# Optimization experiments

Hardware: AMD Instinct MI355X
Metric: run time of the kernel (lower is better)

The kernel has to match this reference:

```python
import jax, jax.numpy as jnp
import numpy as np

D_MODEL = 1024
NUM_HEADS = 16
D_FF = 2688
BATCH = 2
SEQ = 2048
EPS = 1e-5


def _trunc_normal(key, shape, std):
    # truncated normal on [-3, 3] then scaled by std (matches trunc_normal_(mean=0,std,a=-3,b=3) approximately)
    return std * jax.random.truncated_normal(key, -3.0 / std if std > 0 else -3.0, 3.0 / std if std > 0 else 3.0, shape, jnp.float32) * std / std if False else jax.random.truncated_normal(key, -3.0, 3.0, shape, jnp.float32) * std


def setup_inputs() -> dict:
    key = jax.random.key(0)
    ks = jax.random.split(key, 8)
    def lin(k, d_out, d_in):
        std = (2.0 / (d_in + d_out)) ** 0.5
        return _trunc_normal(k, (d_out, d_in), std)
    return {
        "x": jax.random.normal(ks[0], (BATCH, SEQ, D_MODEL), jnp.float32),
        "wqkv": lin(ks[1], 3 * D_MODEL, D_MODEL),
        "wo": lin(ks[2], D_MODEL, D_MODEL),
        "g1": jnp.ones((D_MODEL,), jnp.float32),
        "g2": jnp.ones((D_MODEL,), jnp.float32),
        "w1": lin(ks[3], D_FF, D_MODEL),
        "w2": lin(ks[4], D_MODEL, D_FF),
        "w3": lin(ks[5], D_FF, D_MODEL),
    }


def _rmsnorm(x, g):
    rms = jnp.sqrt(jnp.mean(x * x, axis=-1, keepdims=True) + EPS)
    return x * (g / rms)


def _mhsa(x, wqkv, wo):
    B, S, D = x.shape
    H, Dk = NUM_HEADS, D // NUM_HEADS
    qkv = jnp.einsum('bsd,ed->bse', x, wqkv)  # [B,S,3D]
    q, k, v = jnp.split(qkv, 3, axis=-1)
    def heads(t):
        return t.reshape(B, S, H, Dk).transpose(0, 2, 1, 3)  # [B,H,S,Dk]
    q, k, v = heads(q), heads(k), heads(v)
    scores = jnp.einsum('bhqd,bhkd->bhqk', q, k) / jnp.sqrt(jnp.asarray(Dk, x.dtype))
    causal = jnp.tril(jnp.ones((S, S), bool))
    scores = jnp.where(causal, scores, -jnp.inf)
    attn = jax.nn.softmax(scores, axis=-1)
    out = jnp.einsum('bhqk,bhkd->bhqd', attn, v)
    out = out.transpose(0, 2, 1, 3).reshape(B, S, D)
    return jnp.einsum('bsd,ed->bse', out, wo)


def _swiglu(x, w1, w2, w3):
    a = jnp.einsum('bsd,fd->bsf', x, w1)
    b = jnp.einsum('bsd,fd->bsf', x, w3)
    h = (a * jax.nn.sigmoid(a)) * b
    return jnp.einsum('bsf,df->bsd', h, w2)


def reference(x, wqkv, wo, g1, g2, w1, w2, w3):
    x = x + _mhsa(_rmsnorm(x, g1), wqkv, wo)
    x = x + _swiglu(_rmsnorm(x, g2), w1, w2, w3)
    return x
```

## Files before the change

### kernel.cpp

```cpp
#include <hip/hip_runtime.h>
#include <cstdint>
#include <cstddef>

typedef unsigned short u16;
typedef __attribute__((ext_vector_type(8))) short short8;
typedef __attribute__((ext_vector_type(4))) float float4v;

struct alignas(8) u16x4 { u16 x, y, z, w; };

__device__ __forceinline__ float bf2f(u16 u) {
  union { uint32_t i; float f; } x;
  x.i = ((uint32_t)u) << 16;
  return x.f;
}
__device__ __forceinline__ u16 f2bf(float f) {
  union { float f; uint32_t i; } x;
  x.f = f;
  uint32_t r = x.i + 0x7fffu + ((x.i >> 16) & 1u);
  return (u16)(r >> 16);
}
__device__ __forceinline__ int4 pack8(const float4& a, const float4& b) {
  int4 r;
  r.x = (uint32_t)f2bf(a.x) | ((uint32_t)f2bf(a.y) << 16);
  r.y = (uint32_t)f2bf(a.z) | ((uint32_t)f2bf(a.w) << 16);
  r.z = (uint32_t)f2bf(b.x) | ((uint32_t)f2bf(b.y) << 16);
  r.w = (uint32_t)f2bf(b.z) | ((uint32_t)f2bf(b.w) << 16);
  return r;
}

__device__ __forceinline__ void gload_lds16(const void* g, void* l) {
  __builtin_amdgcn_global_load_lds(
      (const __attribute__((address_space(1))) void*)g,
      (__attribute__((address_space(3))) void*)l, 16, 0, 0);
}

__device__ __forceinline__ int2 xcd_swizzle_xmajor() {
  const int gx = gridDim.x, gy = gridDim.y;
  const int nwg = gx * gy;
  const int lin = blockIdx.x + blockIdx.y * gx;
  const int nl = (lin & 7) * (nwg >> 3) + (lin >> 3);
  const int bx = nl / gy;
  const int by = nl - bx * gy;
  return make_int2(bx, by);
}

struct PrepArgs {
  const float* src[5];
  u16* dst[5];
  int pre[6];
};

__global__ __launch_bounds__(256) void prep_kernel(PrepArgs a)
{
  const int g = blockIdx.x * 256 + threadIdx.x;
  if (g >= a.pre[5]) return;
  int t = 0;
#pragma unroll
  for (int i = 0; i < 5; i++) if (g >= a.pre[i + 1]) t = i + 1;
  const int idx = (g - a.pre[t]) * 8;
  const float* s = a.src[t] + idx;
  float4 v0 = *(const float4*)(s);
  float4 v1 = *(const float4*)(s + 4);
  *(int4*)(a.dst[t] + idx) = pack8(v0, v1);
}

template <int RMODE, bool OUTF32, int TN>
__global__ __launch_bounds__(256) void gemm_bt_kernel(
    const u16* __restrict__ A, const u16* __restrict__ B,
    void* __restrict__ Cv, const void* __restrict__ Rv,
    int M, int N, int K)
{
  constexpr int JN = TN / 32;
  __shared__ u16 As[2][128 * 32];
  __shared__ u16 Bs[2][TN * 32];
  const int t = threadIdx.x;
  const int lane = t & 63;
  const int wave = t >> 6;
  const int l15 = lane & 15;
  const int quad = lane >> 4;
  const int wm = (wave >> 1) * 64;
  const int wn = (wave & 1) * (TN / 2);
  const int2 bb = xcd_swizzle_xmajor();
  const int m0 = bb.y * 128;
  const int n0 = bb.x * TN;
  const int sw = quad ^ ((l15 >> 1) & 3);

  float4v acc[4][JN] = {};

  const int r0 = t >> 2, q0s = (t & 3) ^ ((t >> 3) & 3);
  const int s1 = 256 + t;
  const int r1 = s1 >> 2, q1s = (s1 & 3) ^ ((s1 >> 3) & 3);

  auto stage = [&](int bi, int kk) {
    gload_lds16(A + (size_t)(m0 + r0) * K + kk + q0s * 8, &As[bi][(wave * 64) * 8]);
    gload_lds16(A + (size_t)(m0 + r1) * K + kk + q1s * 8, &As[bi][(256 + wave * 64) * 8]);
    gload_lds16(B + (size_t)(n0 + r0) * K + kk + q0s * 8, &Bs[bi][(wave * 64) * 8]);
    if (TN == 128)
      gload_lds16(B + (size_t)(n0 + r1) * K + kk + q1s * 8, &Bs[bi][(256 + wave * 64) * 8]);
  };
  auto compute = [&](int bi) {
    short8 af[4], bfr[JN];
#pragma unroll
    for (int i = 0; i < 4; i++)
      af[i] = *(const short8*)(&As[bi][((wm + i * 16 + l15) * 4 + sw) * 8]);
#pragma unroll
    for (int j = 0; j < JN; j++)
      bfr[j] = *(const short8*)(&Bs[bi][((wn + j * 16 + l15) * 4 + sw) * 8]);
#pragma unroll
    for (int i = 0; i < 4; i++)
#pragma unroll
      for (int j = 0; j < JN; j++)
        acc[i][j] = __builtin_amdgcn_mfma_f32_16x16x32_bf16(af[i], bfr[j], acc[i][j], 0, 0, 0);
  };

  stage(0, 0);
  __syncthreads();
  for (int kk = 0; kk < K; kk += 64) {
    stage(1, kk + 32);
    compute(0);
    __syncthreads();
    if (kk + 64 < K) stage(0, kk + 64);
    compute(1);
    __syncthreads();
  }

#pragma unroll
  for (int i = 0; i < 4; i++) {
#pragma unroll
    for (int r = 0; r < 4; r++) {
      const int row = m0 + wm + i * 16 + quad * 4 + r;
      const size_t base = (size_t)row * N;
#pragma unroll
      for (int j = 0; j < JN; j++) {
        const int col = n0 + wn + j * 16 + l15;
        float v = acc[i][j][r];
        if (RMODE == 1) v += ((const float*)Rv)[base + col];
        if (RMODE == 2) v += bf2f(((const u16*)Rv)[base + col]);
        if (OUTF32) ((float*)Cv)[base + col] = v;
        else        ((u16*)Cv)[base + col] = f2bf(v);
      }
    }
  }
}

__global__ __launch_bounds__(256) void gemm_w13_kernel(
    const u16* __restrict__ A, const u16* __restrict__ B1,
    const u16* __restrict__ B2, u16* __restrict__ C,
    int M, int N, int K)
{
  __shared__ u16 As[2][128 * 32];
  __shared__ u16 B1s[2][64 * 32];
  __shared__ u16 B2s[2][64 * 32];
  const int t = threadIdx.x;
  const int lane = t & 63;
  const int wave = t >> 6;
  const int l15 = lane & 15;
  const int quad = lane >> 4;
  const int wm = (wave >> 1) * 64;
  const int wn = (wave & 1) * 32;
  const int2 bb = xcd_swizzle_xmajor();
  const int m0 = bb.y * 128;
  const int n0 = bb.x * 64;
  const int sw = quad ^ ((l15 >> 1) & 3);

  float4v accA[4][2] = {};
  float4v accB[4][2] = {};

  const int r0 = t >> 2, q0s = (t & 3) ^ ((t >> 3) & 3);
  const int s1 = 256 + t;
  const int r1 = s1 >> 2, q1s = (s1 & 3) ^ ((s1 >> 3) & 3);

  auto stage = [&](int bi, int kk) {
    gload_lds16(A + (size_t)(m0 + r0) * K + kk + q0s * 8, &As[bi][(wave * 64) * 8]);
    gload_lds16(A + (size_t)(m0 + r1) * K + kk + q1s * 8, &As[bi][(256 + wave * 64) * 8]);
    gload_lds16(B1 + (size_t)(n0 + r0) * K + kk + q0s * 8, &B1s[bi][(wave * 64) * 8]);
    gload_lds16(B2 + (size_t)(n0 + r0) * K + kk + q0s * 8, &B2s[bi][(wave * 64) * 8]);
  };
  auto compute = [&](int bi) {
    short8 af[4], b1f[2], b2f[2];
#pragma unroll
    for (int i = 0; i < 4; i++)
      af[i] = *(const short8*)(&As[bi][((wm + i * 16 + l15) * 4 + sw) * 8]);
#pragma unroll
    for (int j = 0; j < 2; j++) {
      b1f[j] = *(const short8*)(&B1s[bi][((wn + j * 16 + l15) * 4 + sw) * 8]);
      b2f[j] = *(const short8*)(&B2s[bi][((wn + j * 16 + l15) * 4 + sw) * 8]);
    }
#pragma unroll
    for (int i = 0; i < 4; i++)
#pragma unroll
      for (int j = 0; j < 2; j++) {
        accA[i][j] = __builtin_amdgcn_mfma_f32_16x16x32_bf16(af[i], b1f[j], accA[i][j], 0, 0, 0);
        accB[i][j] = __builtin_amdgcn_mfma_f32_16x16x32_bf16(af[i], b2f[j], accB[i][j], 0, 0, 0);
      }
  };

  stage(0, 0);
  __syncthreads();
  for (int kk = 0; kk < K; kk += 64) {
    stage(1, kk + 32);
    compute(0);
    __syncthreads();
    if (kk + 64 < K) stage(0, kk + 64);
    compute(1);
    __syncthreads();
  }

#pragma unroll
  for (int i = 0; i < 4; i++) {
#pragma unroll
    for (int r = 0; r < 4; r++) {
      const int row = m0 + wm + i * 16 + quad * 4 + r;
      const size_t base = (size_t)row * N;
#pragma unroll
      for (int j = 0; j < 2; j++) {
        const int col = n0 + wn + j * 16 + l15;
        float a = accA[i][j][r];
        float b = accB[i][j][r];
        float h = a / (1.f + __expf(-a)) * b;
        C[base + col] = f2bf(h);
      }
    }
  }
}

__global__ __launch_bounds__(256) void vtrans_kernel(
    const u16* __restrict__ qkv, u16* __restrict__ VtG)
{
  __shared__ u16 T[64 * 72];
  const int t = threadIdx.x;
  const int s0 = blockIdx.x * 64;
  const int bh = blockIdx.y, b = bh >> 4, h = bh & 15;
  {
    const int sl = t >> 2, dseg = (t & 3) * 16;
    const size_t src = ((size_t)b * 2048 + s0 + sl) * 3072 + 2048 + h * 64 + dseg;
    int4 v0 = *(const int4*)(qkv + src);
    int4 v1 = *(const int4*)(qkv + src + 8);
    *(int4*)(&T[sl * 72 + dseg]) = v0;
    *(int4*)(&T[sl * 72 + dseg + 8]) = v1;
  }
  __syncthreads();
  {
    const int d = t >> 2, sseg = (t & 3) * 16;
    alignas(16) u16 buf[16];
#pragma unroll
    for (int i = 0; i < 16; i++) buf[i] = T[(sseg + i) * 72 + d];
    u16* dst = VtG + ((size_t)bh * 64 + d) * 2048 + s0 + sseg;
    *(int4*)(dst) = *(const int4*)(&buf[0]);
    *(int4*)(dst + 8) = *(const int4*)(&buf[8]);
  }
}

__global__ __launch_bounds__(256) void attn_kernel(
    const u16* __restrict__ qkv, const u16* __restrict__ VtG,
    u16* __restrict__ outp)
{
  __shared__ u16 Ks[2][128 * 32];
  __shared__ u16 Vt[4][64 * 32];
  __shared__ u16 Pl[4][2048];
  const int t = threadIdx.x;
  const int lane = t & 63;
  const int wave = t >> 6;
  const int l15 = lane & 15;
  const int quad = lane >> 4;
  const int sw = quad ^ ((l15 >> 1) & 3);
  const int gx = gridDim.x;
  const int nwg = gx * gridDim.y;
  const int lin = blockIdx.x + blockIdx.y * gx;
  const int nl = (lin & 7) * (nwg >> 3) + (lin >> 3);
  const int bh = nl / gx;
  const int pair = nl - bh * gx;
  const int b = bh >> 4, h = bh & 15;
  const size_t srow = (size_t)b * 2048;
  const int rr = lane >> 2, qs = (lane & 3) ^ ((lane >> 3) & 3);
  u16* plw = Pl[wave];

  for (int tsel = 0; tsel < 2; tsel++) {
    const int qt = tsel ? 31 - pair : pair;
    const int tq0 = qt * 64;
    const int q = tq0 + wave * 16 + l15;

    short8 qf[2];
    {
      const size_t qbase = (srow + q) * 3072 + h * 64;
#pragma unroll
      for (int dh = 0; dh < 2; dh++) {
        int4 raw = *(const int4*)(qkv + qbase + dh * 32 + quad * 8);
        const u16* rp = (const u16*)&raw;
        short8 f;
#pragma unroll
        for (int j = 0; j < 8; j++)
          ((u16*)&f)[j] = f2bf(bf2f(rp[j]) * 0.125f);
        qf[dh] = f;
      }
    }

    float m_i = -INFINITY, l_i = 0.f;
    float4v accO[4] = {};
    const int nc = (qt + 2) >> 1;

    for (int ic = 0; ic < nc; ic++) {
      const int c0 = ic * 128;
#pragma unroll
      for (int k = 0; k < 8; k++) {
        const int I = wave * 8 + k;
        if (I < 16) {
          const int half = I >> 3, rb = (I & 7) * 16, row = rb + rr;
          gload_lds16(qkv + (srow + c0 + row) * 3072 + 1024 + h * 64 + half * 32 + qs * 8,
                      &Ks[half][rb * 32]);
        } else {
          const int g = (I - 16) >> 2, rb = ((I - 16) & 3) * 16, row = rb + rr;
          gload_lds16(VtG + ((size_t)bh * 64 + row) * 2048 + c0 + g * 32 + qs * 8,
                      &Vt[g][rb * 32]);
        }
      }
      __syncthreads();

      float4v accS[8];
#pragma unroll
      for (int ks = 0; ks < 8; ks++) {
        short8 kf0 = *(const short8*)(&Ks[0][((ks * 16 + l15) * 4 + sw) * 8]);
        short8 kf1 = *(const short8*)(&Ks[1][((ks * 16 + l15) * 4 + sw) * 8]);
        float4v z = {};
        z = __builtin_amdgcn_mfma_f32_16x16x32_bf16(kf0, qf[0], z, 0, 0, 0);
        accS[ks] = __builtin_amdgcn_mfma_f32_16x16x32_bf16(kf1, qf[1], z, 0, 0, 0);
      }

      if (ic == nc - 1) {
#pragma unroll
        for (int ks = 0; ks < 8; ks++)
#pragma unroll
          for (int r = 0; r < 4; r++)
            if (c0 + ks * 16 + quad * 4 + r > q) accS[ks][r] = -INFINITY;
      }

      float cmax = -INFINITY;
#pragma unroll
      for (int ks = 0; ks < 8; ks++)
#pragma unroll
        for (int r = 0; r < 4; r++) cmax = fmaxf(cmax, accS[ks][r]);
      cmax = fmaxf(cmax, __shfl_xor(cmax, 16));
      cmax = fmaxf(cmax, __shfl_xor(cmax, 32));
      const float mn = fmaxf(m_i, cmax);
      const float alpha = __expf(m_i - mn);

      float psum = 0.f;
#pragma unroll
      for (int ks = 0; ks < 8; ks++) {
        float p0 = __expf(accS[ks][0] - mn);
        float p1 = __expf(accS[ks][1] - mn);
        float p2 = __expf(accS[ks][2] - mn);
        float p3 = __expf(accS[ks][3] - mn);
        psum += (p0 + p1) + (p2 + p3);
        u16x4 pk;
        pk.x = f2bf(p0); pk.y = f2bf(p1); pk.z = f2bf(p2); pk.w = f2bf(p3);
        const int seg = ((ks & 1) * 2 + (quad >> 1)) ^ ((l15 >> 1) & 3);
        *(u16x4*)(&plw[(ks >> 1) * 512 + (l15 * 4 + seg) * 8 + (quad & 1) * 4]) = pk;
      }
      psum += __shfl_xor(psum, 16);
      psum += __shfl_xor(psum, 32);
      l_i = l_i * alpha + psum;
      m_i = mn;
#pragma unroll
      for (int ds = 0; ds < 4; ds++)
#pragma unroll
        for (int r = 0; r < 4; r++) accO[ds][r] *= alpha;

      __threadfence_block();

#pragma unroll
      for (int kh = 0; kh < 4; kh++) {
        short8 pf = *(const short8*)(&plw[kh * 512 + (l15 * 4 + sw) * 8]);
#pragma unroll
        for (int ds = 0; ds < 4; ds++) {
          short8 vf = *(const short8*)(&Vt[kh][((ds * 16 + l15) * 4 + sw) * 8]);
          accO[ds] = __builtin_amdgcn_mfma_f32_16x16x32_bf16(vf, pf, accO[ds], 0, 0, 0);
        }
      }
      __syncthreads();
    }

    const float invl = 1.f / l_i;
    const size_t obase = (srow + q) * 1024 + h * 64;
#pragma unroll
    for (int ds = 0; ds < 4; ds++) {
      u16x4 pk;
      pk.x = f2bf(accO[ds][0] * invl);
      pk.y = f2bf(accO[ds][1] * invl);
      pk.z = f2bf(accO[ds][2] * invl);
      pk.w = f2bf(accO[ds][3] * invl);
      *(u16x4*)(outp + obase + ds * 16 + quad * 4) = pk;
    }
  }
}

template <bool XF32>
__global__ __launch_bounds__(256) void rmsnorm_kernel(
    const void* __restrict__ xv, const float* __restrict__ g, u16* __restrict__ o)
{
  const int row = blockIdx.x;
  const int t = threadIdx.x;
  float f0, f1, f2, f3;
  if (XF32) {
    float4 v = *(const float4*)((const float*)xv + (size_t)row * 1024 + t * 4);
    f0 = v.x; f1 = v.y; f2 = v.z; f3 = v.w;
  } else {
    int2 v = *(const int2*)((const u16*)xv + (size_t)row * 1024 + t * 4);
    const u16* p = (const u16*)&v;
    f0 = bf2f(p[0]); f1 = bf2f(p[1]); f2 = bf2f(p[2]); f3 = bf2f(p[3]);
  }
  float ss = f0 * f0 + f1 * f1 + f2 * f2 + f3 * f3;
#pragma unroll
  for (int off = 32; off > 0; off >>= 1) ss += __shfl_down(ss, off);
  __shared__ float red[4];
  if ((t & 63) == 0) red[t >> 6] = ss;
  __syncthreads();
  const float tot = red[0] + red[1] + red[2] + red[3];
  const float inv = rsqrtf(tot * (1.0f / 1024.0f) + 1e-5f);
  float4 gv = *(const float4*)(g + t * 4);
  u16x4 ov;
  ov.x = f2bf(f0 * gv.x * inv);
  ov.y = f2bf(f1 * gv.y * inv);
  ov.z = f2bf(f2 * gv.z * inv);
  ov.w = f2bf(f3 * gv.w * inv);
  *(u16x4*)(o + (size_t)row * 1024 + t * 4) = ov;
}

extern "C" void kernel_launch(void* const* d_in, const int* in_sizes, int n_in,
                              void* d_out, int out_size, void* d_ws, size_t ws_size,
                              hipStream_t stream)
{
  const float* x    = (const float*)d_in[0];
  const float* wqkv = (const float*)d_in[1];
  const float* wo   = (const float*)d_in[2];
  const float* g1   = (const float*)d_in[3];
  const float* g2   = (const float*)d_in[4];
  const float* w1   = (const float*)d_in[5];
  const float* w2   = (const float*)d_in[6];
  const float* w3   = (const float*)d_in[7];
  float* out = (float*)d_out;
  char* ws = (char*)d_ws;
  (void)in_sizes; (void)n_in; (void)out_size; (void)ws_size;

  size_t off = 0;
  auto alloc = [&](size_t bytes) { void* p = ws + off; off += (bytes + 255) & ~(size_t)255; return p; };
  u16* wqkvb = (u16*)alloc((size_t)3072 * 1024 * 2);
  u16* wob   = (u16*)alloc((size_t)1024 * 1024 * 2);
  u16* w1b   = (u16*)alloc((size_t)2688 * 1024 * 2);
  u16* w2b   = (u16*)alloc((size_t)2688 * 1024 * 2);
  u16* w3b   = (u16*)alloc((size_t)2688 * 1024 * 2);
  u16* S1    = (u16*)alloc((size_t)4096 * 1024 * 2);
  u16* S2    = (u16*)alloc((size_t)4096 * 3072 * 2);
  u16* S3    = (u16*)alloc((size_t)4096 * 1024 * 2);
  u16* VtG   = (u16*)alloc((size_t)32 * 64 * 2048 * 2);

  PrepArgs pa;
  const float* srcs[5] = {wqkv, wo, w1, w2, w3};
  u16* dsts[5] = {wqkvb, wob, w1b, w2b, w3b};
  const int nelem[5] = {3072 * 1024, 1024 * 1024, 2688 * 1024, 2688 * 1024, 2688 * 1024};
  int pre = 0;
  for (int i = 0; i < 5; i++) {
    pa.src[i] = srcs[i];
    pa.dst[i] = dsts[i];
    pa.pre[i] = pre;
    pre += nelem[i] / 8;
  }
  pa.pre[5] = pre;
  prep_kernel<<<(pre + 255) / 256, 256, 0, stream>>>(pa);

  rmsnorm_kernel<true><<<4096, 256, 0, stream>>>(x, g1, S1);
  gemm_bt_kernel<0, false, 128><<<dim3(24, 32), 256, 0, stream>>>(S1, wqkvb, S2,
                                                  nullptr, 4096, 3072, 1024);
  vtrans_kernel<<<dim3(32, 32), 256, 0, stream>>>(S2, VtG);
  attn_kernel<<<dim3(16, 32), 256, 0, stream>>>(S2, VtG, S1);
  gemm_bt_kernel<1, false, 64><<<dim3(16, 32), 256, 0, stream>>>(S1, wob, S3, x,
                                                  4096, 1024, 1024);
  rmsnorm_kernel<false><<<4096, 256, 0, stream>>>(S3, g2, S1);
  gemm_w13_kernel<<<dim3(42, 32), 256, 0, stream>>>(S1, w1b, w3b, S2,
                                                  4096, 2688, 1024);
  gemm_bt_kernel<2, true, 64><<<dim3(16, 32), 256, 0, stream>>>(S2, w2b, out, S3,
                                                  4096, 1024, 2688);
}
```

Before: 339.6 us.

## Triple-buffer GEMM K-loop and double-buffer attention KV with partial vmcnt waits

The GEMM and fused W1/W3 kernels move from a two-stage LDS pipeline to three stages. Each iteration issues the load two steps ahead and waits with an explicit s_waitcnt vmcnt count, so only the oldest tile must arrive before the barrier. The attention kernel double-buffers its K and V tiles, prefetching the next chunk while computing the current one. This should hide global-to-LDS latency in exchange for more LDS per block, which may lower occupancy, and it relies on hand-counted vmcnt values being correct.

```diff
diff --git a/kernel.cpp b/kernel.cpp
--- a/kernel.cpp
+++ b/kernel.cpp
@@ -33,6 +33,20 @@
       (const __attribute__((address_space(1))) void*)g,
       (__attribute__((address_space(3))) void*)l, 16, 0, 0);
 }
+
+#define WAITV_BAR(N)                                              \
+  do {                                                            \
+    asm volatile("s_waitcnt vmcnt(%0)" ::"n"(N) : "memory");      \
+    __builtin_amdgcn_s_barrier();                                 \
+    __builtin_amdgcn_sched_barrier(0);                            \
+  } while (0)
+
+#define BAR_ONLY()                                                \
+  do {                                                            \
+    __builtin_amdgcn_sched_barrier(0);                            \
+    __builtin_amdgcn_s_barrier();                                 \
+    __builtin_amdgcn_sched_barrier(0);                            \
+  } while (0)
 
 __device__ __forceinline__ int2 xcd_swizzle_xmajor() {
   const int gx = gridDim.x, gy = gridDim.y;
@@ -71,8 +85,9 @@
     int M, int N, int K)
 {
   constexpr int JN = TN / 32;
-  __shared__ u16 As[2][128 * 32];
-  __shared__ u16 Bs[2][TN * 32];
+  constexpr int NLD = (TN == 128) ? 4 : 3;
+  __shared__ u16 As[3][128 * 32];
+  __shared__ u16 Bs[3][TN * 32];
   const int t = threadIdx.x;
   const int lane = t & 63;
   const int wave = t >> 6;
@@ -113,16 +128,23 @@
         acc[i][j] = __builtin_amdgcn_mfma_f32_16x16x32_bf16(af[i], bfr[j], acc[i][j], 0, 0, 0);
   };
 
+  const int nk = K >> 5;
   stage(0, 0);
-  __syncthreads();
-  for (int kk = 0; kk < K; kk += 64) {
-    stage(1, kk + 32);
-    compute(0);
-    __syncthreads();
-    if (kk + 64 < K) stage(0, kk + 64);
-    compute(1);
-    __syncthreads();
-  }
+  stage(1, 32);
+  int bc = 0, bs = 2;
+  for (int i = 0; i + 2 < nk; ++i) {
+    stage(bs, (i + 2) << 5);
+    WAITV_BAR(2 * NLD);
+    compute(bc);
+    BAR_ONLY();
+    bc = (bc == 2) ? 0 : bc + 1;
+    bs = (bs == 2) ? 0 : bs + 1;
+  }
+  WAITV_BAR(NLD);
+  compute(bc);
+  bc = (bc == 2) ? 0 : bc + 1;
+  WAITV_BAR(0);
+  compute(bc);
 
 #pragma unroll
   for (int i = 0; i < 4; i++) {
@@ -148,9 +170,9 @@
     const u16* __restrict__ B2, u16* __restrict__ C,
     int M, int N, int K)
 {
-  __shared__ u16 As[2][128 * 32];
-  __shared__ u16 B1s[2][64 * 32];
-  __shared__ u16 B2s[2][64 * 32];
+  __shared__ u16 As[3][128 * 32];
+  __shared__ u16 B1s[3][64 * 32];
+  __shared__ u16 B2s[3][64 * 32];
   const int t = threadIdx.x;
   const int lane = t & 63;
   const int wave = t >> 6;
@@ -195,16 +217,23 @@
       }
   };
 
+  const int nk = K >> 5;
   stage(0, 0);
-  __syncthreads();
-  for (int kk = 0; kk < K; kk += 64) {
-    stage(1, kk + 32);
-    compute(0);
-    __syncthreads();
-    if (kk + 64 < K) stage(0, kk + 64);
-    compute(1);
-    __syncthreads();
-  }
+  stage(1, 32);
+  int bc = 0, bs = 2;
+  for (int i = 0; i + 2 < nk; ++i) {
+    stage(bs, (i + 2) << 5);
+    WAITV_BAR(8);
+    compute(bc);
+    BAR_ONLY();
+    bc = (bc == 2) ? 0 : bc + 1;
+    bs = (bs == 2) ? 0 : bs + 1;
+  }
+  WAITV_BAR(4);
+  compute(bc);
+  bc = (bc == 2) ? 0 : bc + 1;
+  WAITV_BAR(0);
+  compute(bc);
 
 #pragma unroll
   for (int i = 0; i < 4; i++) {
@@ -255,8 +284,8 @@
     const u16* __restrict__ qkv, const u16* __restrict__ VtG,
     u16* __restrict__ outp)
 {
-  __shared__ u16 Ks[2][128 * 32];
-  __shared__ u16 Vt[4][64 * 32];
+  __shared__ u16 Ks[2][2][128 * 32];
+  __shared__ u16 Vt[2][4][64 * 32];
   __shared__ u16 Pl[4][2048];
   const int t = threadIdx.x;
   const int lane = t & 63;
@@ -275,6 +304,23 @@
   const int rr = lane >> 2, qs = (lane & 3) ^ ((lane >> 3) & 3);
   u16* plw = Pl[wave];
 
+  auto stageKV = [&](int bi, int ic) {
+    const int c0 = ic * 128;
+#pragma unroll
+    for (int k = 0; k < 8; k++) {
+      const int I = wave * 8 + k;
+      if (I < 16) {
+        const int half = I >> 3, rb = (I & 7) * 16, row = rb + rr;
+        gload_lds16(qkv + (srow + c0 + row) * 3072 + 1024 + h * 64 + half * 32 + qs * 8,
+                    &Ks[bi][half][rb * 32]);
+      } else {
+        const int g = (I - 16) >> 2, rb = ((I - 16) & 3) * 16, row = rb + rr;
+        gload_lds16(VtG + ((size_t)bh * 64 + row) * 2048 + c0 + g * 32 + qs * 8,
+                    &Vt[bi][g][rb * 32]);
+      }
+    }
+  };
+
   for (int tsel = 0; tsel < 2; tsel++) {
     const int qt = tsel ? 31 - pair : pair;
     const int tq0 = qt * 64;
@@ -299,28 +345,22 @@
     float4v accO[4] = {};
     const int nc = (qt + 2) >> 1;
 
+    stageKV(0, 0);
     for (int ic = 0; ic < nc; ic++) {
+      const int cb = ic & 1;
       const int c0 = ic * 128;
-#pragma unroll
-      for (int k = 0; k < 8; k++) {
-        const int I = wave * 8 + k;
-        if (I < 16) {
-          const int half = I >> 3, rb = (I & 7) * 16, row = rb + rr;
-          gload_lds16(qkv + (srow + c0 + row) * 3072 + 1024 + h * 64 + half * 32 + qs * 8,
-                      &Ks[half][rb * 32]);
-        } else {
-          const int g = (I - 16) >> 2, rb = ((I - 16) & 3) * 16, row = rb + rr;
-          gload_lds16(VtG + ((size_t)bh * 64 + row) * 2048 + c0 + g * 32 + qs * 8,
-                      &Vt[g][rb * 32]);
-        }
-      }
-      __syncthreads();
+      if (ic + 1 < nc) {
+        stageKV(cb ^ 1, ic + 1);
+        WAITV_BAR(8);
+      } else {
+        WAITV_BAR(0);
+      }
 
       float4v accS[8];
 #pragma unroll
       for (int ks = 0; ks < 8; ks++) {
-        short8 kf0 = *(const short8*)(&Ks[0][((ks * 16 + l15) * 4 + sw) * 8]);
-        short8 kf1 = *(const short8*)(&Ks[1][((ks * 16 + l15) * 4 + sw) * 8]);
+        short8 kf0 = *(const short8*)(&Ks[cb][0][((ks * 16 + l15) * 4 + sw) * 8]);
+        short8 kf1 = *(const short8*)(&Ks[cb][1][((ks * 16 + l15) * 4 + sw) * 8]);
         float4v z = {};
         z = __builtin_amdgcn_mfma_f32_16x16x32_bf16(kf0, qf[0], z, 0, 0, 0);
         accS[ks] = __builtin_amdgcn_mfma_f32_16x16x32_bf16(kf1, qf[1], z, 0, 0, 0);
@@ -373,11 +413,11 @@
         short8 pf = *(const short8*)(&plw[kh * 512 + (l15 * 4 + sw) * 8]);
 #pragma unroll
         for (int ds = 0; ds < 4; ds++) {
-          short8 vf = *(const short8*)(&Vt[kh][((ds * 16 + l15) * 4 + sw) * 8]);
+          short8 vf = *(const short8*)(&Vt[cb][kh][((ds * 16 + l15) * 4 + sw) * 8]);
           accO[ds] = __builtin_amdgcn_mfma_f32_16x16x32_bf16(vf, pf, accO[ds], 0, 0, 0);
         }
       }
-      __syncthreads();
+      BAR_ONLY();
     }
 
     const float invl = 1.f / l_i;
```

New measurement: 326.7 us. 1.04x faster.
